# Kernel tuning notes

Measured on AMD Instinct MI355X. Metric: run time of the kernel, lower is better.

The kernel has to match this reference:

```python
import jax, jax.numpy as jnp
import numpy as np
import math

# B graphs of exactly NMAX nodes each
N, B, NMAX, E = 131072, 256, 512, 1048576
F_IN, C, H, HEADS, NUM_CLASSES = 128, 32, 64, 4, 2
K1 = 128  # ceil(avg_num_nodes * pooling_ratio) = ceil(512 * 0.25)
SCALE = math.sqrt(H)  # GMT MAB scales by sqrt(dim_V), not sqrt(head_dim)


def gcn_conv(x, W, b, src, dst, n):
    h = x @ W
    deg = jax.ops.segment_sum(jnp.ones(dst.shape[0], x.dtype), dst, num_segments=n) + 1.0
    dinv = jax.lax.rsqrt(deg)
    msg = h[src] * (dinv[src] * dinv[dst])[:, None]
    out = jax.ops.segment_sum(msg, dst, num_segments=n)
    out = out + h * (dinv * dinv)[:, None]  # self-loop term
    return out + b


def mab(Qin, K, V, addmask, Wq, bq, Wo, bo):
    # GMT multihead attention block (layer_norm=False)
    Q = Qin @ Wq + bq
    b_, nq, _ = Q.shape
    dh = H // HEADS
    q = Q.reshape(b_, nq, HEADS, dh)
    k = K.reshape(b_, K.shape[1], HEADS, dh)
    v = V.reshape(b_, K.shape[1], HEADS, dh)
    s = jnp.einsum('bqhd,bkhd->bhqk', q, k) / SCALE
    if addmask is not None:
        s = s + addmask[:, None, None, :]  # mask invalid keys
    A = jax.nn.softmax(s, axis=-1)
    o = jnp.einsum('bhqk,bkhd->bqhd', A, v).reshape(b_, nq, H)
    o = Q + o
    return o + jax.nn.relu(o @ Wo + bo)


def _forward(x0, conv1_W, conv1_b, conv2_W, conv2_b, conv3_W, conv3_b,
             pool_lin1_W, pool_lin1_b,
             pma1_S, pma1_Wq, pma1_bq, pma1_Wk, pma1_bk, pma1_Wv, pma1_bv, pma1_Wo, pma1_bo,
             sab_Wq, sab_bq, sab_Wk, sab_bk, sab_Wv, sab_bv, sab_Wo, sab_bo,
             pma2_S, pma2_Wq, pma2_bq, pma2_Wk, pma2_bk, pma2_Wv, pma2_bv, pma2_Wo, pma2_bo,
             pool_lin2_W, pool_lin2_b, lin1_W, lin1_b, lin2_W, lin2_b,
             edge_index, batch):
    src, dst = edge_index[0], edge_index[1]
    x1 = jax.nn.relu(gcn_conv(x0, conv1_W, conv1_b, src, dst, N))
    x2 = jax.nn.relu(gcn_conv(x1, conv2_W, conv2_b, src, dst, N))
    x3 = jax.nn.relu(gcn_conv(x2, conv3_W, conv3_b, src, dst, N))
    xc = jnp.concatenate([x1, x2, x3], axis=-1)         # [N, 96]
    xl = xc @ pool_lin1_W + pool_lin1_b                 # [N, H] (GMT lin1)

    # to_dense_batch bookkeeping (batch is sorted per graph)
    counts = jax.ops.segment_sum(jnp.ones(N, jnp.int32), batch, num_segments=B)
    starts = jnp.cumsum(counts) - counts
    pos = jnp.arange(N, dtype=jnp.int32) - starts[batch]
    valid = jnp.zeros((B, NMAX), bool).at[batch, pos].set(True)
    addmask = jnp.where(valid, 0.0, -1e9).astype(xl.dtype)

    def dense(h):
        return jnp.zeros((B, NMAX, h.shape[-1]), h.dtype).at[batch, pos].set(h)

    # GMPool_G: seed queries attend over GCNConv-transformed node features
    Kd = dense(gcn_conv(xl, pma1_Wk, pma1_bk, src, dst, N))
    Vd = dense(gcn_conv(xl, pma1_Wv, pma1_bv, src, dst, N))
    Q = jnp.broadcast_to(pma1_S[None], (B, K1, H))
    bx = mab(Q, Kd, Vd, addmask, pma1_Wq, pma1_bq, pma1_Wo, pma1_bo)

    # SelfAtt (mask=None after first pool)
    bx = mab(bx, bx @ sab_Wk + sab_bk, bx @ sab_Wv + sab_bv, None,
             sab_Wq, sab_bq, sab_Wo, sab_bo)

    # GMPool_I with single seed (last pool -> 1 output node per graph)
    Q2 = jnp.broadcast_to(pma2_S[None], (B, 1, H))
    bx = mab(Q2, bx @ pma2_Wk + pma2_bk, bx @ pma2_Wv + pma2_bv, None,
             pma2_Wq, pma2_bq, pma2_Wo, pma2_bo)

    g = bx[:, 0] @ pool_lin2_W + pool_lin2_b            # [B, 32] (GMT lin2)
    h1 = jax.nn.relu(g @ lin1_W + lin1_b)               # dropout identity in eval
    logits = h1 @ lin2_W + lin2_b
    return jax.nn.log_softmax(logits, axis=-1)


def setup_inputs() -> dict:
    key = jax.random.key(0)
    ks = iter(jax.random.split(key, 80))
    def Wm(fi, fo):
        return jax.random.normal(next(ks), (fi, fo), jnp.float32) / np.sqrt(fi)
    def bv(fo):
        return jax.random.normal(next(ks), (fo,), jnp.float32) * 0.01
    inp = {}
    inp['x0'] = jax.random.normal(next(ks), (N, F_IN), jnp.float32)
    g = jax.random.randint(next(ks), (E,), 0, B)
    so = jax.random.randint(next(ks), (E,), 0, NMAX)
    do = jax.random.randint(next(ks), (E,), 0, NMAX)
    inp['edge_index'] = jnp.stack([g * NMAX + so, g * NMAX + do]).astype(jnp.int32)
    inp['batch'] = jnp.arange(N, dtype=jnp.int32) // NMAX
    inp['conv1_W'], inp['conv1_b'] = Wm(F_IN, C), bv(C)
    inp['conv2_W'], inp['conv2_b'] = Wm(C, C), bv(C)
    inp['conv3_W'], inp['conv3_b'] = Wm(C, C), bv(C)
    inp['pool_lin1_W'], inp['pool_lin1_b'] = Wm(3 * C, H), bv(H)
    inp['pma1_S'] = jax.random.normal(next(ks), (K1, H), jnp.float32)
    for p in ['pma1', 'sab', 'pma2']:
        for nm in ['q', 'k', 'v', 'o']:
            inp[p + '_W' + nm], inp[p + '_b' + nm] = Wm(H, H), bv(H)
    inp['pma2_S'] = jax.random.normal(next(ks), (1, H), jnp.float32)
    inp['pool_lin2_W'], inp['pool_lin2_b'] = Wm(H, C), bv(C)
    inp['lin1_W'], inp['lin1_b'] = Wm(C, 16), bv(16)
    inp['lin2_W'], inp['lin2_b'] = Wm(16, NUM_CLASSES), bv(NUM_CLASSES)
    return inp


def reference(x0, edge_index, batch, conv1_W, conv1_b, conv2_W, conv2_b, conv3_W, conv3_b,
              pool_lin1_W, pool_lin1_b,
              pma1_S, pma1_Wq, pma1_bq, pma1_Wk, pma1_bk, pma1_Wv, pma1_bv, pma1_Wo, pma1_bo,
              sab_Wq, sab_bq, sab_Wk, sab_bk, sab_Wv, sab_bv, sab_Wo, sab_bo,
              pma2_S, pma2_Wq, pma2_bq, pma2_Wk, pma2_bk, pma2_Wv, pma2_bv, pma2_Wo, pma2_bo,
              pool_lin2_W, pool_lin2_b, lin1_W, lin1_b, lin2_W, lin2_b):
    return _forward(x0, conv1_W, conv1_b, conv2_W, conv2_b, conv3_W, conv3_b,
                    pool_lin1_W, pool_lin1_b,
                    pma1_S, pma1_Wq, pma1_bq, pma1_Wk, pma1_bk, pma1_Wv, pma1_bv, pma1_Wo, pma1_bo,
                    sab_Wq, sab_bq, sab_Wk, sab_bk, sab_Wv, sab_bv, sab_Wo, sab_bo,
                    pma2_S, pma2_Wq, pma2_bq, pma2_Wk, pma2_bk, pma2_Wv, pma2_bv, pma2_Wo, pma2_bo,
                    pool_lin2_W, pool_lin2_b, lin1_W, lin1_b, lin2_W, lin2_b,
                    edge_index, batch)
```

## Files before the change

### kernel.cpp

```cpp
#include <hip/hip_runtime.h>
#include <hip/hip_bf16.h>

#define N_NODES 131072
#define NGRAPH  256
#define NMAXN   512
#define NEDGE   1048576
#define FIN     128
#define HDIM    64
#define K1Q     128
#define EPB     1024
#define NBLK    (NEDGE / EPB)

__global__ __launch_bounds__(256) void k_hist2(const int* __restrict__ dst,
                                               int* __restrict__ h) {
    __shared__ int lh[NGRAPH];
    const int tid = threadIdx.x;
    lh[tid] = 0;
    __syncthreads();
    const int base = blockIdx.x * EPB;
#pragma unroll
    for (int j = 0; j < 4; ++j)
        atomicAdd(&lh[dst[base + j * 256 + tid] >> 9], 1);
    __syncthreads();
    h[blockIdx.x * 256 + tid] = lh[tid];
}

__global__ __launch_bounds__(256) void k_scan_bins(int* __restrict__ h,
                                                   int* __restrict__ binTot) {
    const int b = blockIdx.x;
    const int tid = threadIdx.x;
    int v[4], s = 0;
#pragma unroll
    for (int j = 0; j < 4; ++j) { v[j] = h[(tid * 4 + j) * 256 + b]; s += v[j]; }
    __shared__ int sc[256];
    sc[tid] = s;
    __syncthreads();
    for (int o = 1; o < 256; o <<= 1) {
        int t = (tid >= o) ? sc[tid - o] : 0;
        __syncthreads();
        sc[tid] += t;
        __syncthreads();
    }
    int run = sc[tid] - s;
#pragma unroll
    for (int j = 0; j < 4; ++j) { int t = v[j]; h[(tid * 4 + j) * 256 + b] = run; run += t; }
    if (tid == 255) binTot[b] = sc[255];
}

__global__ __launch_bounds__(256) void k_binstart(const int* __restrict__ binTot,
                                                  int* __restrict__ starts) {
    const int tid = threadIdx.x;
    int v = binTot[tid];
    __shared__ int sc[256];
    sc[tid] = v;
    __syncthreads();
    for (int o = 1; o < 256; o <<= 1) {
        int t = (tid >= o) ? sc[tid - o] : 0;
        __syncthreads();
        sc[tid] += t;
        __syncthreads();
    }
    starts[tid] = sc[tid] - v;
    if (tid == 255) starts[256] = sc[255];
}

__global__ __launch_bounds__(256) void k_scatter2(const int* __restrict__ src,
                                                  const int* __restrict__ dst,
                                                  const int* __restrict__ h,
                                                  const int* __restrict__ starts,
                                                  int* __restrict__ epack) {
    __shared__ int base[NGRAPH];
    const int tid = threadIdx.x;
    base[tid] = h[blockIdx.x * 256 + tid] + starts[tid];
    __syncthreads();
    const int b0 = blockIdx.x * EPB;
#pragma unroll
    for (int j = 0; j < 4; ++j) {
        int e = b0 + j * 256 + tid;
        int d = dst[e];
        int pos = atomicAdd(&base[d >> 9], 1);
        epack[pos] = ((src[e] & (NMAXN - 1)) << 9) | (d & (NMAXN - 1));
    }
}

__global__ __launch_bounds__(256) void k_sort_dst(
    const int* __restrict__ epack, const int* __restrict__ starts,
    int* __restrict__ esrc, int* __restrict__ rowptr)
{
    __shared__ int hist[NMAXN];
    __shared__ int excl[NMAXN];
    __shared__ int psc[256];
    const int g = blockIdx.x, tid = threadIdx.x;
    const int e0 = starts[g], e1 = starts[g + 1];
    hist[tid] = 0; hist[tid + 256] = 0;
    __syncthreads();
    for (int e = e0 + tid; e < e1; e += 256)
        atomicAdd(&hist[epack[e] & (NMAXN - 1)], 1);
    __syncthreads();
    int a = hist[2 * tid], b = hist[2 * tid + 1];
    psc[tid] = a + b;
    __syncthreads();
    for (int o = 1; o < 256; o <<= 1) {
        int t = (tid >= o) ? psc[tid - o] : 0;
        __syncthreads();
        psc[tid] += t;
        __syncthreads();
    }
    int ep = psc[tid] - a - b;
    excl[2 * tid] = ep;
    excl[2 * tid + 1] = ep + a;
    __syncthreads();
    rowptr[g * NMAXN + 2 * tid]     = e0 + excl[2 * tid];
    rowptr[g * NMAXN + 2 * tid + 1] = e0 + excl[2 * tid + 1];
    if (g == NGRAPH - 1 && tid == 0) rowptr[N_NODES] = NEDGE;
    __syncthreads();
    for (int e = e0 + tid; e < e1; e += 256) {
        int p = epack[e];
        int d = p & (NMAXN - 1);
        int pos = e0 + atomicAdd(&excl[d], 1);
        esrc[pos] = p >> 9;
    }
}

__global__ void k_dinv2(const int* __restrict__ rowptr, float* __restrict__ d) {
    int i = blockIdx.x * blockDim.x + threadIdx.x;
    if (i < N_NODES) d[i] = rsqrtf((float)(rowptr[i + 1] - rowptr[i]) + 1.0f);
}

template<int TM, int K, int CO, int MODE>
__global__ __launch_bounds__(256) void k_gemm(
    const float* __restrict__ A, int lda,
    const float* __restrict__ W, const float* __restrict__ bias,
    float* __restrict__ out, int ldo, int M)
{
    constexpr int WTS = K + 4;
    __shared__ float As[TM * K];
    __shared__ float Wt[CO * WTS];
    const int tid = threadIdx.x;
    const int row0 = blockIdx.x * TM;

    for (int i = tid; i < K * CO; i += 256) {
        int k = i / CO, c = i - k * CO;
        Wt[c * WTS + k] = W[i];
    }
    constexpr int VR = K / 4;
    for (int i = tid; i < TM * VR; i += 256) {
        int r = i / VR, v = i - r * VR;
        int gr = row0 + r;
        float4 val = make_float4(0.f, 0.f, 0.f, 0.f);
        if (gr < M) val = *(const float4*)(A + (size_t)gr * lda + v * 4);
        *(float4*)(As + r * K + v * 4) = val;
    }
    __syncthreads();

    constexpr int G = 256 / CO;
    constexpr int RPT = TM / G;
    const int co = tid % CO;
    const int g = tid / CO;

    float acc[RPT];
#pragma unroll
    for (int r = 0; r < RPT; ++r) acc[r] = 0.f;

    const float* wrow = Wt + co * WTS;
    for (int kk = 0; kk < K / 4; ++kk) {
        float4 w = *(const float4*)(wrow + kk * 4);
#pragma unroll
        for (int r = 0; r < RPT; ++r) {
            float4 a = *(const float4*)(As + (g * RPT + r) * K + kk * 4);
            acc[r] += a.x * w.x + a.y * w.y + a.z * w.z + a.w * w.w;
        }
    }
    float b = 0.f;
    if (MODE >= 1) b = bias[co];
#pragma unroll
    for (int r = 0; r < RPT; ++r) {
        int gr = row0 + g * RPT + r;
        if (gr < M) {
            float v = acc[r] + b;
            if (MODE == 2) v = fmaxf(v, 0.f);
            out[(size_t)gr * ldo + co] = v;
        }
    }
}

template<int RELU>
__global__ __launch_bounds__(256) void k_gcn_agg2(
    const float* __restrict__ T, int ldt,
    const float* __restrict__ dinv, const float* __restrict__ bias,
    const int* __restrict__ esrc, const int* __restrict__ rowptr,
    float* __restrict__ out, int ldo)
{
    constexpr int LS = 36;
    __shared__ float Tl[NMAXN * LS];
    __shared__ float dl[NMAXN];
    const int g = blockIdx.x;
    const int tid = threadIdx.x;
    const int node0 = g * NMAXN;

    for (int i = tid; i < NMAXN; i += 256) dl[i] = dinv[node0 + i];
    __syncthreads();
    for (int i = tid; i < NMAXN * 8; i += 256) {
        int r = i >> 3, c4 = (i & 7) << 2;
        float4 v = *(const float4*)(T + (size_t)(node0 + r) * ldt + c4);
        float w = dl[r];
        v.x *= w; v.y *= w; v.z *= w; v.w *= w;
        *(float4*)(Tl + r * LS + c4) = v;
    }
    __syncthreads();
    for (int i = tid; i < NMAXN * 8; i += 256) {
        int n = i >> 3, c4 = (i & 7) << 2;
        float4 acc = *(const float4*)(Tl + n * LS + c4);
        const int eb = rowptr[node0 + n], ee = rowptr[node0 + n + 1];
        for (int e = eb; e < ee; ++e) {
            int ls = esrc[e];
            const float4 v = *(const float4*)(Tl + ls * LS + c4);
            acc.x += v.x; acc.y += v.y; acc.z += v.z; acc.w += v.w;
        }
        float w = dl[n];
        float4 b4 = *(const float4*)(bias + c4);
        float4 o;
        o.x = b4.x + w * acc.x; o.y = b4.y + w * acc.y;
        o.z = b4.z + w * acc.z; o.w = b4.w + w * acc.w;
        if (RELU) {
            o.x = fmaxf(o.x, 0.f); o.y = fmaxf(o.y, 0.f);
            o.z = fmaxf(o.z, 0.f); o.w = fmaxf(o.w, 0.f);
        }
        *(float4*)(out + (size_t)(node0 + n) * ldo + c4) = o;
    }
}

template<int NK, bool QSH>
__global__ __launch_bounds__(256) void k_attn(
    const float* __restrict__ Q, const float* __restrict__ K,
    const float* __restrict__ V, float* __restrict__ O)
{
    constexpr int KH = NK / 2;
    __shared__ float Ks[NK * 16];
    __shared__ float Vs[NK * 16];
    __shared__ float Ml[128 * 18];
    const int g = blockIdx.x >> 2;
    const int h = blockIdx.x & 3;
    const int tid = threadIdx.x;
    for (int i = tid; i < NK * 4; i += 256) {
        int k = i >> 2, dc = (i & 3) << 2;
        const size_t off = ((size_t)g * NK + k) * HDIM + h * 16 + dc;
        *(float4*)(Ks + k * 16 + dc) = *(const float4*)(K + off);
        *(float4*)(Vs + k * 16 + dc) = *(const float4*)(V + off);
    }
    __syncthreads();
    const int q = tid & 127;
    const int half = tid >> 7;
    const int k0 = half * KH;
    const float* qp = QSH ? (Q + (size_t)q * HDIM + h * 16)
                          : (Q + ((size_t)g * K1Q + q) * HDIM + h * 16);
    float qv[16];
#pragma unroll
    for (int d = 0; d < 16; ++d) qv[d] = qp[d];

    float m = -1e30f, l = 0.f;
    float acc[16];
#pragma unroll
    for (int d = 0; d < 16; ++d) acc[d] = 0.f;

    for (int kt = 0; kt < KH; kt += 8) {
        const int kb = k0 + kt;
        float s[8];
#pragma unroll
        for (int j = 0; j < 8; ++j) {
            float t = 0.f;
#pragma unroll
            for (int d4 = 0; d4 < 4; ++d4) {
                float4 kv = *(const float4*)(Ks + (kb + j) * 16 + d4 * 4);
                t += qv[d4*4] * kv.x + qv[d4*4+1] * kv.y
                   + qv[d4*4+2] * kv.z + qv[d4*4+3] * kv.w;
            }
            s[j] = t * 0.125f;
        }
        float tmax = fmaxf(fmaxf(fmaxf(s[0], s[1]), fmaxf(s[2], s[3])),
                           fmaxf(fmaxf(s[4], s[5]), fmaxf(s[6], s[7])));
        if (tmax > m + 8.f) {
            float cr = __expf(m - tmax);
            l *= cr;
#pragma unroll
            for (int d = 0; d < 16; ++d) acc[d] *= cr;
            m = tmax;
        }
        float p[8];
#pragma unroll
        for (int j = 0; j < 8; ++j) { p[j] = __expf(s[j] - m); l += p[j]; }
#pragma unroll
        for (int d4 = 0; d4 < 4; ++d4) {
#pragma unroll
            for (int j = 0; j < 8; ++j) {
                float4 v = *(const float4*)(Vs + (kb + j) * 16 + d4 * 4);
                acc[d4*4]   += p[j] * v.x;
                acc[d4*4+1] += p[j] * v.y;
                acc[d4*4+2] += p[j] * v.z;
                acc[d4*4+3] += p[j] * v.w;
            }
        }
    }
    if (half) {
        float* w = Ml + q * 18;
        w[0] = m; w[1] = l;
#pragma unroll
        for (int d = 0; d < 16; ++d) w[2 + d] = acc[d];
    }
    __syncthreads();
    if (!half) {
        const float* r = Ml + q * 18;
        float m1 = r[0], l1 = r[1];
        float M = fmaxf(m, m1);
        float c0 = __expf(m - M), c1 = __expf(m1 - M);
        float inv = 1.f / (l * c0 + l1 * c1);
        float* op = O + ((size_t)g * K1Q + q) * HDIM + h * 16;
#pragma unroll
        for (int d = 0; d < 16; ++d) op[d] = (acc[d] * c0 + r[2 + d] * c1) * inv;
    }
}

__global__ __launch_bounds__(256) void k_attn_pma2(
    const float* __restrict__ Q2p, const float* __restrict__ K3,
    const float* __restrict__ V3, float* __restrict__ O3)
{
    const int t = threadIdx.x;
    const int lane = t & 63;
    const int g = blockIdx.x * 4 + (t >> 6);
    const float q = Q2p[lane];
    const float* Kg = K3 + (size_t)g * 128 * HDIM + lane;
    const float* Vg = V3 + (size_t)g * 128 * HDIM + lane;
    float m = -1e30f, l = 0.f, acc = 0.f;
    for (int k = 0; k < 128; ++k) {
        float s = q * Kg[(size_t)k * HDIM];
        s += __shfl_xor(s, 1); s += __shfl_xor(s, 2);
        s += __shfl_xor(s, 4); s += __shfl_xor(s, 8);
        s *= 0.125f;
        float mn = fmaxf(m, s);
        float cr = __expf(m - mn), p = __expf(s - mn);
        l = l * cr + p;
        acc = acc * cr + p * Vg[(size_t)k * HDIM];
        m = mn;
    }
    O3[(size_t)g * HDIM + lane] = acc / l;
}

template<int NQ>
__global__ __launch_bounds__(256) void k_mab_epi(
    const float* __restrict__ AO, const float* __restrict__ Qsrc,
    const float* __restrict__ W, const float* __restrict__ bias,
    float* __restrict__ out, int M)
{
    constexpr int TM = 128, KK = 64, CO = 64, WTS = KK + 4;
    __shared__ float Os[TM * KK];
    __shared__ float Wt[CO * WTS];
    const int tid = threadIdx.x;
    const int row0 = blockIdx.x * TM;
    for (int i = tid; i < KK * CO; i += 256) {
        int k = i >> 6, c = i & 63;
        Wt[c * WTS + k] = W[i];
    }
    for (int i = tid; i < TM * 16; i += 256) {
        int r = i >> 4, v = (i & 15) << 2;
        int gr = row0 + r;
        float4 a = make_float4(0.f, 0.f, 0.f, 0.f);
        if (gr < M) {
            float4 x = *(const float4*)(AO + (size_t)gr * KK + v);
            int qr = (NQ == 0) ? gr : (NQ == 1 ? 0 : (gr & (NQ - 1)));
            float4 qv = *(const float4*)(Qsrc + (size_t)qr * KK + v);
            a.x = x.x + qv.x; a.y = x.y + qv.y; a.z = x.z + qv.z; a.w = x.w + qv.w;
        }
        *(float4*)(Os + r * KK + v) = a;
    }
    __syncthreads();
    const int co = tid & 63, g = tid >> 6;
    float acc[32];
#pragma unroll
    for (int r = 0; r < 32; ++r) acc[r] = 0.f;
    const float* wrow = Wt + co * WTS;
    for (int kk = 0; kk < KK / 4; ++kk) {
        float4 w = *(const float4*)(wrow + kk * 4);
#pragma unroll
        for (int r = 0; r < 32; ++r) {
            float4 a = *(const float4*)(Os + (g * 32 + r) * KK + kk * 4);
            acc[r] += a.x * w.x + a.y * w.y + a.z * w.z + a.w * w.w;
        }
    }
    float b = bias[co];
#pragma unroll
    for (int r = 0; r < 32; ++r) {
        int gr = row0 + g * 32 + r;
        if (gr < M) {
            float o = Os[(g * 32 + r) * KK + co];
            out[(size_t)gr * CO + co] = o + fmaxf(acc[r] + b, 0.f);
        }
    }
}

__global__ __launch_bounds__(64) void k_head(
    const float* __restrict__ BX3,
    const float* __restrict__ W1, const float* __restrict__ b1,
    const float* __restrict__ W2, const float* __restrict__ b2,
    const float* __restrict__ W3, const float* __restrict__ b3,
    float* __restrict__ outp)
{
    __shared__ float w1[64 * 32], w2[32 * 16], w3[32], bb1[32], bb2[16], bb3[2];
    const int tid = threadIdx.x;
    for (int i = tid; i < 64 * 32; i += 64) w1[i] = W1[i];
    for (int i = tid; i < 32 * 16; i += 64) w2[i] = W2[i];
    if (tid < 32) { w3[tid] = W3[tid]; bb1[tid] = b1[tid]; }
    if (tid < 16) bb2[tid] = b2[tid];
    if (tid < 2)  bb3[tid] = b3[tid];
    __syncthreads();
    const int g = blockIdx.x * 64 + tid;
    float x[64];
#pragma unroll
    for (int v = 0; v < 16; ++v) {
        float4 t = *(const float4*)(BX3 + (size_t)g * 64 + v * 4);
        x[v*4] = t.x; x[v*4+1] = t.y; x[v*4+2] = t.z; x[v*4+3] = t.w;
    }
    float gv[32];
    for (int c = 0; c < 32; ++c) {
        float a = bb1[c];
        for (int k = 0; k < 64; ++k) a += x[k] * w1[k * 32 + c];
        gv[c] = a;
    }
    float h1[16];
    for (int c = 0; c < 16; ++c) {
        float a = bb2[c];
        for (int k = 0; k < 32; ++k) a += gv[k] * w2[k * 16 + c];
        h1[c] = fmaxf(a, 0.f);
    }
    float z0 = bb3[0], z1 = bb3[1];
    for (int k = 0; k < 16; ++k) { z0 += h1[k] * w3[k * 2]; z1 += h1[k] * w3[k * 2 + 1]; }
    float mm = fmaxf(z0, z1);
    float ls = mm + logf(__expf(z0 - mm) + __expf(z1 - mm));
    outp[g * 2]     = z0 - ls;
    outp[g * 2 + 1] = z1 - ls;
}

extern "C" void kernel_launch(void* const* d_in, const int* in_sizes, int n_in,
                              void* d_out, int out_size, void* d_ws, size_t ws_size,
                              hipStream_t stream) {
    const float* x0  = (const float*)d_in[0];
    const int*   ei  = (const int*)d_in[1];
    const float* c1W = (const float*)d_in[3];  const float* c1b = (const float*)d_in[4];
    const float* c2W = (const float*)d_in[5];  const float* c2b = (const float*)d_in[6];
    const float* c3W = (const float*)d_in[7];  const float* c3b = (const float*)d_in[8];
    const float* plW = (const float*)d_in[9];  const float* plb = (const float*)d_in[10];
    const float* S1  = (const float*)d_in[11];
    const float* p1Wq = (const float*)d_in[12]; const float* p1bq = (const float*)d_in[13];
    const float* p1Wk = (const float*)d_in[14]; const float* p1bk = (const float*)d_in[15];
    const float* p1Wv = (const float*)d_in[16]; const float* p1bv = (const float*)d_in[17];
    const float* p1Wo = (const float*)d_in[18]; const float* p1bo = (const float*)d_in[19];
    const float* sWq  = (const float*)d_in[20]; const float* sbq  = (const float*)d_in[21];
    const float* sWk  = (const float*)d_in[22]; const float* sbk  = (const float*)d_in[23];
    const float* sWv  = (const float*)d_in[24]; const float* sbv  = (const float*)d_in[25];
    const float* sWo  = (const float*)d_in[26]; const float* sbo  = (const float*)d_in[27];
    const float* p2Wq = (const float*)d_in[28]; const float* p2bq = (const float*)d_in[29];
    const float* p2Wk = (const float*)d_in[30]; const float* p2bk = (const float*)d_in[31];
    const float* p2Wv = (const float*)d_in[32]; const float* p2bv = (const float*)d_in[33];
    const float* p2Wo = (const float*)d_in[34]; const float* p2bo = (const float*)d_in[35];
    const float* S2   = (const float*)d_in[36];
    const float* pl2W = (const float*)d_in[37]; const float* pl2b = (const float*)d_in[38];
    const float* l1W  = (const float*)d_in[39]; const float* l1b  = (const float*)d_in[40];
    const float* l2W  = (const float*)d_in[41]; const float* l2b  = (const float*)d_in[42];

    const int* src = ei;
    const int* dst = ei + NEDGE;

    float* ws = (float*)d_ws;
    float* dinv = ws;
    size_t off = N_NODES;
    int* epack  = (int*)(ws + off); off += NEDGE;
    int* h      = (int*)(ws + off); off += NBLK * 256;
    int* binTot = (int*)(ws + off); off += 256;
    int* starts = (int*)(ws + off); off += 257;
    int* esrc   = (int*)(ws + off); off += NEDGE;
    int* rowptr = (int*)(ws + off); off += N_NODES + 1;
    off = (off + 255) & ~(size_t)255;
    float* Qp  = ws + off; off += K1Q * HDIM;
    float* Q2p = ws + off; off += HDIM;
    float* O3  = ws + off; off += NGRAPH * HDIM;
    float* BX3 = ws + off; off += NGRAPH * HDIM;
    off = (off + 1023) & ~(size_t)1023;
    float* P0 = ws + off;
    const size_t SL = (size_t)N_NODES * 32;
    float* T32 = P0;
    float* T64 = P0;
    float* XC  = P0 + 2 * SL;
    float* XL  = P0 + 5 * SL;
    float* KD  = P0 + 2 * SL;
    float* VD  = P0 + 5 * SL;
    float* O1  = P0 + 4 * SL;
    float* BX1 = P0 + 4 * SL + SL / 2;
    float* Qs  = P0;
    float* Ks_ = P0 + SL / 2;
    float* Vs_ = P0 + SL;
    float* O2  = P0 + SL + SL / 2;
    float* BX2 = P0 + 2 * SL;
    float* K3  = P0 + 2 * SL + SL / 2;
    float* V3  = P0 + 3 * SL;

    k_hist2<<<NBLK, 256, 0, stream>>>(dst, h);
    k_scan_bins<<<256, 256, 0, stream>>>(h, binTot);
    k_binstart<<<1, 256, 0, stream>>>(binTot, starts);
    k_scatter2<<<NBLK, 256, 0, stream>>>(src, dst, h, starts, epack);
    k_sort_dst<<<NGRAPH, 256, 0, stream>>>(epack, starts, esrc, rowptr);
    k_dinv2<<<512, 256, 0, stream>>>(rowptr, dinv);

    k_gemm<64, 128, 32, 0><<<2048, 256, 0, stream>>>(x0, FIN, c1W, nullptr, T32, 32, N_NODES);
    k_gcn_agg2<1><<<256, 256, 0, stream>>>(T32, 32, dinv, c1b, esrc, rowptr, XC, 96);
    k_gemm<128, 32, 32, 0><<<1024, 256, 0, stream>>>(XC, 96, c2W, nullptr, T32, 32, N_NODES);
    k_gcn_agg2<1><<<256, 256, 0, stream>>>(T32, 32, dinv, c2b, esrc, rowptr, XC + 32, 96);
    k_gemm<128, 32, 32, 0><<<1024, 256, 0, stream>>>(XC + 32, 96, c3W, nullptr, T32, 32, N_NODES);
    k_gcn_agg2<1><<<256, 256, 0, stream>>>(T32, 32, dinv, c3b, esrc, rowptr, XC + 64, 96);

    k_gemm<64, 96, 64, 1><<<2048, 256, 0, stream>>>(XC, 96, plW, plb, XL, 64, N_NODES);

    k_gemm<128, 64, 64, 0><<<1024, 256, 0, stream>>>(XL, 64, p1Wk, nullptr, T64, 64, N_NODES);
    k_gcn_agg2<0><<<256, 256, 0, stream>>>(T64, 64, dinv, p1bk, esrc, rowptr, KD, 64);
    k_gcn_agg2<0><<<256, 256, 0, stream>>>(T64 + 32, 64, dinv, p1bk + 32, esrc, rowptr, KD + 32, 64);
    k_gemm<128, 64, 64, 0><<<1024, 256, 0, stream>>>(XL, 64, p1Wv, nullptr, T64, 64, N_NODES);
    k_gcn_agg2<0><<<256, 256, 0, stream>>>(T64, 64, dinv, p1bv, esrc, rowptr, VD, 64);
    k_gcn_agg2<0><<<256, 256, 0, stream>>>(T64 + 32, 64, dinv, p1bv + 32, esrc, rowptr, VD + 32, 64);

    k_gemm<128, 64, 64, 1><<<1, 256, 0, stream>>>(S1, 64, p1Wq, p1bq, Qp, 64, K1Q);
    k_attn<512, true><<<NGRAPH * 4, 256, 0, stream>>>(Qp, KD, VD, O1);
    k_mab_epi<128><<<256, 256, 0, stream>>>(O1, Qp, p1Wo, p1bo, BX1, NGRAPH * K1Q);

    k_gemm<128, 64, 64, 1><<<256, 256, 0, stream>>>(BX1, 64, sWq, sbq, Qs, 64, NGRAPH * K1Q);
    k_gemm<128, 64, 64, 1><<<256, 256, 0, stream>>>(BX1, 64, sWk, sbk, Ks_, 64, NGRAPH * K1Q);
    k_gemm<128, 64, 64, 1><<<256, 256, 0, stream>>>(BX1, 64, sWv, sbv, Vs_, 64, NGRAPH * K1Q);
    k_attn<128, false><<<NGRAPH * 4, 256, 0, stream>>>(Qs, Ks_, Vs_, O2);
    k_mab_epi<0><<<256, 256, 0, stream>>>(O2, Qs, sWo, sbo, BX2, NGRAPH * K1Q);

    k_gemm<128, 64, 64, 1><<<256, 256, 0, stream>>>(BX2, 64, p2Wk, p2bk, K3, 64, NGRAPH * K1Q);
    k_gemm<128, 64, 64, 1><<<256, 256, 0, stream>>>(BX2, 64, p2Wv, p2bv, V3, 64, NGRAPH * K1Q);
    k_gemm<128, 64, 64, 1><<<1, 256, 0, stream>>>(S2, 64, p2Wq, p2bq, Q2p, 64, 1);
    k_attn_pma2<<<64, 256, 0, stream>>>(Q2p, K3, V3, O3);
    k_mab_epi<1><<<2, 256, 0, stream>>>(O3, Q2p, p2Wo, p2bo, BX3, NGRAPH);

    k_head<<<4, 64, 0, stream>>>(BX3, pl2W, pl2b, l1W, l1b, l2W, l2b,
                                 (float*)d_out);
}
```

Before: 1.182 ms.

## Fuse GCN feature GEMM into per-graph aggregation and split attention keys four ways

Replaces the separate node-feature GEMM plus aggregation kernels with one per-graph kernel. It stages the input rows and transposed weights in shared memory, computes the 32-column projection in registers, then aggregates over neighbours from shared memory. This removes the round trip of the intermediate T tensor through global memory and several launches. The attention kernel now splits keys into four quarters, with each thread handling two queries and a four-way merge that reuses the K buffer when it is large enough. The costs are a 64-entry register accumulator that may hurt occupancy, and only 256 blocks for the fused GEMM work.

```diff
diff --git a/kernel.cpp b/kernel.cpp
--- a/kernel.cpp
+++ b/kernel.cpp
@@ -184,44 +184,79 @@
     }
 }
 
-template<int RELU>
-__global__ __launch_bounds__(256) void k_gcn_agg2(
-    const float* __restrict__ T, int ldt,
-    const float* __restrict__ dinv, const float* __restrict__ bias,
+template<int K, int RELU>
+__global__ __launch_bounds__(256) void k_gcn_fused(
+    const float* __restrict__ A, int lda,
+    const float* __restrict__ W, int ldw,
+    const float* __restrict__ bias,
+    const float* __restrict__ dinv,
     const int* __restrict__ esrc, const int* __restrict__ rowptr,
     float* __restrict__ out, int ldo)
 {
-    constexpr int LS = 36;
-    __shared__ float Tl[NMAXN * LS];
+    constexpr int C   = 8192 / K;
+    constexpr int NCH = NMAXN / C;
+    constexpr int RPT = C / 8;
+    constexpr int LS  = 36;
+    constexpr int WTS = K + 4;
+    __shared__ float U[NMAXN * LS];
     __shared__ float dl[NMAXN];
-    const int g = blockIdx.x;
-    const int tid = threadIdx.x;
+    float* As = U;
+    float* Wt = U + 8192;
+    const int g = blockIdx.x, tid = threadIdx.x;
     const int node0 = g * NMAXN;
 
+    for (int i = tid; i < 32 * K; i += 256) {
+        int k = i >> 5, co = i & 31;
+        Wt[co * WTS + k] = W[k * ldw + co];
+    }
     for (int i = tid; i < NMAXN; i += 256) dl[i] = dinv[node0 + i];
-    __syncthreads();
-    for (int i = tid; i < NMAXN * 8; i += 256) {
-        int r = i >> 3, c4 = (i & 7) << 2;
-        float4 v = *(const float4*)(T + (size_t)(node0 + r) * ldt + c4);
-        float w = dl[r];
-        v.x *= w; v.y *= w; v.z *= w; v.w *= w;
-        *(float4*)(Tl + r * LS + c4) = v;
-    }
+
+    const int co = tid & 31, grp = tid >> 5;
+    float acc[64];
+#pragma unroll
+    for (int r = 0; r < 64; ++r) acc[r] = 0.f;
+
+#pragma unroll
+    for (int ch = 0; ch < NCH; ++ch) {
+        __syncthreads();
+        for (int i = tid; i < C * (K / 4); i += 256) {
+            int r = i / (K / 4), v = i % (K / 4);
+            *(float4*)(As + r * K + v * 4) =
+                *(const float4*)(A + (size_t)(node0 + ch * C + r) * lda + v * 4);
+        }
+        __syncthreads();
+        for (int kk = 0; kk < K / 4; ++kk) {
+            float4 w = *(const float4*)(Wt + co * WTS + kk * 4);
+#pragma unroll
+            for (int r = 0; r < RPT; ++r) {
+                float4 a = *(const float4*)(As + (grp * RPT + r) * K + kk * 4);
+                acc[ch * RPT + r] += a.x * w.x + a.y * w.y + a.z * w.z + a.w * w.w;
+            }
+        }
+    }
+    __syncthreads();
+    float* Tl = U;
+#pragma unroll
+    for (int ch = 0; ch < NCH; ++ch)
+#pragma unroll
+        for (int r = 0; r < RPT; ++r) {
+            int row = ch * C + grp * RPT + r;
+            Tl[row * LS + co] = acc[ch * RPT + r] * dl[row];
+        }
     __syncthreads();
     for (int i = tid; i < NMAXN * 8; i += 256) {
         int n = i >> 3, c4 = (i & 7) << 2;
-        float4 acc = *(const float4*)(Tl + n * LS + c4);
+        float4 s = *(const float4*)(Tl + n * LS + c4);
         const int eb = rowptr[node0 + n], ee = rowptr[node0 + n + 1];
         for (int e = eb; e < ee; ++e) {
-            int ls = esrc[e];
-            const float4 v = *(const float4*)(Tl + ls * LS + c4);
-            acc.x += v.x; acc.y += v.y; acc.z += v.z; acc.w += v.w;
-        }
-        float w = dl[n];
+            const float4 v = *(const float4*)(Tl + esrc[e] * LS + c4);
+            s.x += v.x; s.y += v.y; s.z += v.z; s.w += v.w;
+        }
+        float wv = dl[n];
         float4 b4 = *(const float4*)(bias + c4);
         float4 o;
-        o.x = b4.x + w * acc.x; o.y = b4.y + w * acc.y;
-        o.z = b4.z + w * acc.z; o.w = b4.w + w * acc.w;
+        o.x = b4.x + wv * s.x; o.y = b4.y + wv * s.y;
+        o.z = b4.z + wv * s.z; o.w = b4.w + wv * s.w;
         if (RELU) {
             o.x = fmaxf(o.x, 0.f); o.y = fmaxf(o.y, 0.f);
             o.z = fmaxf(o.z, 0.f); o.w = fmaxf(o.w, 0.f);
@@ -235,10 +270,12 @@
     const float* __restrict__ Q, const float* __restrict__ K,
     const float* __restrict__ V, float* __restrict__ O)
 {
-    constexpr int KH = NK / 2;
+    constexpr int KQ  = NK / 4;
+    constexpr int MLF = 3 * 128 * 18;
     __shared__ float Ks[NK * 16];
     __shared__ float Vs[NK * 16];
-    __shared__ float Ml[128 * 18];
+    __shared__ float Mlsep[(NK * 16 >= MLF) ? 4 : MLF];
+    float* Ml = (NK * 16 >= MLF) ? Ks : Mlsep;
     const int g = blockIdx.x >> 2;
     const int h = blockIdx.x & 3;
     const int tid = threadIdx.x;
@@ -249,74 +286,111 @@
         *(float4*)(Vs + k * 16 + dc) = *(const float4*)(V + off);
     }
     __syncthreads();
-    const int q = tid & 127;
-    const int half = tid >> 7;
-    const int k0 = half * KH;
-    const float* qp = QSH ? (Q + (size_t)q * HDIM + h * 16)
-                          : (Q + ((size_t)g * K1Q + q) * HDIM + h * 16);
-    float qv[16];
-#pragma unroll
-    for (int d = 0; d < 16; ++d) qv[d] = qp[d];
-
-    float m = -1e30f, l = 0.f;
-    float acc[16];
-#pragma unroll
-    for (int d = 0; d < 16; ++d) acc[d] = 0.f;
-
-    for (int kt = 0; kt < KH; kt += 8) {
+    const int qs = tid & 63;
+    const int quarter = tid >> 6;
+    const int k0 = quarter * KQ;
+    const float* qp0 = QSH ? (Q + (size_t)qs * HDIM + h * 16)
+                           : (Q + ((size_t)g * K1Q + qs) * HDIM + h * 16);
+    const float* qp1 = qp0 + 64 * HDIM;
+    float qv0[16], qv1[16];
+#pragma unroll
+    for (int d = 0; d < 16; ++d) { qv0[d] = qp0[d]; qv1[d] = qp1[d]; }
+
+    float m0 = -1e30f, l0 = 0.f, m1 = -1e30f, l1 = 0.f;
+    float acc0[16], acc1[16];
+#pragma unroll
+    for (int d = 0; d < 16; ++d) { acc0[d] = 0.f; acc1[d] = 0.f; }
+
+    for (int kt = 0; kt < KQ; kt += 8) {
         const int kb = k0 + kt;
-        float s[8];
+        float s0[8], s1[8];
 #pragma unroll
         for (int j = 0; j < 8; ++j) {
-            float t = 0.f;
+            float t0 = 0.f, t1 = 0.f;
 #pragma unroll
             for (int d4 = 0; d4 < 4; ++d4) {
                 float4 kv = *(const float4*)(Ks + (kb + j) * 16 + d4 * 4);
-                t += qv[d4*4] * kv.x + qv[d4*4+1] * kv.y
-                   + qv[d4*4+2] * kv.z + qv[d4*4+3] * kv.w;
+                t0 += qv0[d4*4] * kv.x + qv0[d4*4+1] * kv.y
+                    + qv0[d4*4+2] * kv.z + qv0[d4*4+3] * kv.w;
+                t1 += qv1[d4*4] * kv.x + qv1[d4*4+1] * kv.y
+                    + qv1[d4*4+2] * kv.z + qv1[d4*4+3] * kv.w;
             }
-            s[j] = t * 0.125f;
-        }
-        float tmax = fmaxf(fmaxf(fmaxf(s[0], s[1]), fmaxf(s[2], s[3])),
-                           fmaxf(fmaxf(s[4], s[5]), fmaxf(s[6], s[7])));
-        if (tmax > m + 8.f) {
-            float cr = __expf(m - tmax);
-            l *= cr;
-#pragma unroll
-            for (int d = 0; d < 16; ++d) acc[d] *= cr;
-            m = tmax;
-        }
-        float p[8];
-#pragma unroll
-        for (int j = 0; j < 8; ++j) { p[j] = __expf(s[j] - m); l += p[j]; }
+            s0[j] = t0 * 0.125f; s1[j] = t1 * 0.125f;
+        }
+        float tm0 = fmaxf(fmaxf(fmaxf(s0[0], s0[1]), fmaxf(s0[2], s0[3])),
+                          fmaxf(fmaxf(s0[4], s0[5]), fmaxf(s0[6], s0[7])));
+        float tm1 = fmaxf(fmaxf(fmaxf(s1[0], s1[1]), fmaxf(s1[2], s1[3])),
+                          fmaxf(fmaxf(s1[4], s1[5]), fmaxf(s1[6], s1[7])));
+        if (tm0 > m0 + 8.f) {
+            float cr = __expf(m0 - tm0);
+            l0 *= cr;
+#pragma unroll
+            for (int d = 0; d < 16; ++d) acc0[d] *= cr;
+            m0 = tm0;
+        }
+        if (tm1 > m1 + 8.f) {
+            float cr = __expf(m1 - tm1);
+            l1 *= cr;
+#pragma unroll
+            for (int d = 0; d < 16; ++d) acc1[d] *= cr;
+            m1 = tm1;
+        }
+        float p0[8], p1[8];
+#pragma unroll
+        for (int j = 0; j < 8; ++j) {
+            p0[j] = __expf(s0[j] - m0); l0 += p0[j];
+            p1[j] = __expf(s1[j] - m1); l1 += p1[j];
+        }
 #pragma unroll
         for (int d4 = 0; d4 < 4; ++d4) {
 #pragma unroll
             for (int j = 0; j < 8; ++j) {
                 float4 v = *(const float4*)(Vs + (kb + j) * 16 + d4 * 4);
-                acc[d4*4]   += p[j] * v.x;
-                acc[d4*4+1] += p[j] * v.y;
-                acc[d4*4+2] += p[j] * v.z;
-                acc[d4*4+3] += p[j] * v.w;
+                acc0[d4*4]   += p0[j] * v.x;  acc1[d4*4]   += p1[j] * v.x;
+                acc0[d4*4+1] += p0[j] * v.y;  acc1[d4*4+1] += p1[j] * v.y;
+                acc0[d4*4+2] += p0[j] * v.z;  acc1[d4*4+2] += p1[j] * v.z;
+                acc0[d4*4+3] += p0[j] * v.w;  acc1[d4*4+3] += p1[j] * v.w;
             }
         }
     }
-    if (half) {
-        float* w = Ml + q * 18;
-        w[0] = m; w[1] = l;
-#pragma unroll
-        for (int d = 0; d < 16; ++d) w[2 + d] = acc[d];
-    }
-    __syncthreads();
-    if (!half) {
-        const float* r = Ml + q * 18;
-        float m1 = r[0], l1 = r[1];
-        float M = fmaxf(m, m1);
-        float c0 = __expf(m - M), c1 = __expf(m1 - M);
-        float inv = 1.f / (l * c0 + l1 * c1);
-        float* op = O + ((size_t)g * K1Q + q) * HDIM + h * 16;
-#pragma unroll
-        for (int d = 0; d < 16; ++d) op[d] = (acc[d] * c0 + r[2 + d] * c1) * inv;
+    __syncthreads();
+    if (quarter) {
+        float* w0 = Ml + ((quarter - 1) * 128 + qs) * 18;
+        float* w1 = Ml + ((quarter - 1) * 128 + qs + 64) * 18;
+        w0[0] = m0; w0[1] = l0;
+        w1[0] = m1; w1[1] = l1;
+#pragma unroll
+        for (int d = 0; d < 16; ++d) { w0[2 + d] = acc0[d]; w1[2 + d] = acc1[d]; }
+    }
+    __syncthreads();
+    if (quarter == 0) {
+#pragma unroll
+        for (int qq = 0; qq < 2; ++qq) {
+            const int q = qs + qq * 64;
+            float m = qq ? m1 : m0, l = qq ? l1 : l0;
+            float ac[16];
+#pragma unroll
+            for (int d = 0; d < 16; ++d) ac[d] = qq ? acc1[d] : acc0[d];
+            float M = m;
+#pragma unroll
+            for (int p = 0; p < 3; ++p) M = fmaxf(M, Ml[(p * 128 + q) * 18]);
+            float c = __expf(m - M);
+            float L = l * c;
+#pragma unroll
+            for (int d = 0; d < 16; ++d) ac[d] *= c;
+#pragma unroll
+            for (int p = 0; p < 3; ++p) {
+                const float* r = Ml + (p * 128 + q) * 18;
+                float cp = __expf(r[0] - M);
+                L += r[1] * cp;
+#pragma unroll
+                for (int d = 0; d < 16; ++d) ac[d] += r[2 + d] * cp;
+            }
+            float inv = 1.f / L;
+            float* op = O + ((size_t)g * K1Q + q) * HDIM + h * 16;
+#pragma unroll
+            for (int d = 0; d < 16; ++d) op[d] = ac[d] * inv;
+        }
     }
 }
 
@@ -486,12 +560,10 @@
     off = (off + 1023) & ~(size_t)1023;
     float* P0 = ws + off;
     const size_t SL = (size_t)N_NODES * 32;
-    float* T32 = P0;
-    float* T64 = P0;
     float* XC  = P0 + 2 * SL;
     float* XL  = P0 + 5 * SL;
-    float* KD  = P0 + 2 * SL;
-    float* VD  = P0 + 5 * SL;
+    float* KD  = P0;
+    float* VD  = P0 + 2 * SL;
     float* O1  = P0 + 4 * SL;
     float* BX1 = P0 + 4 * SL + SL / 2;
     float* Qs  = P0;
@@ -509,21 +581,16 @@
     k_sort_dst<<<NGRAPH, 256, 0, stream>>>(epack, starts, esrc, rowptr);
     k_dinv2<<<512, 256, 0, stream>>>(rowptr, dinv);
 
-    k_gemm<64, 128, 32, 0><<<2048, 256, 0, stream>>>(x0, FIN, c1W, nullptr, T32, 32, N_NODES);
-    k_gcn_agg2<1><<<256, 256, 0, stream>>>(T32, 32, dinv, c1b, esrc, rowptr, XC, 96);
-    k_gemm<128, 32, 32, 0><<<1024, 256, 0, stream>>>(XC, 96, c2W, nullptr, T32, 32, N_NODES);
-    k_gcn_agg2<1><<<256, 256, 0, stream>>>(T32, 32, dinv, c2b, esrc, rowptr, XC + 32, 96);
-    k_gemm<128, 32, 32, 0><<<1024, 256, 0, stream>>>(XC + 32, 96, c3W, nullptr, T32, 32, N_NODES);
-    k_gcn_agg2<1><<<256, 256, 0, stream>>>(T32, 32, dinv, c3b, esrc, rowptr, XC + 64, 96);
+    k_gcn_fused<128, 1><<<NGRAPH, 256, 0, stream>>>(x0, FIN, c1W, 32, c1b, dinv, esrc, rowptr, XC, 96);
+    k_gcn_fused<32, 1><<<NGRAPH, 256, 0, stream>>>(XC, 96, c2W, 32, c2b, dinv, esrc, rowptr, XC + 32, 96);
+    k_gcn_fused<32, 1><<<NGRAPH, 256, 0, stream>>>(XC + 32, 96, c3W, 32, c3b, dinv, esrc, rowptr, XC + 64, 96);
 
     k_gemm<64, 96, 64, 1><<<2048, 256, 0, stream>>>(XC, 96, plW, plb, XL, 64, N_NODES);
 
-    k_gemm<128, 64, 64, 0><<<1024, 256, 0, stream>>>(XL, 64, p1Wk, nullptr, T64, 64, N_NODES);
-    k_gcn_agg2<0><<<256, 256, 0, stream>>>(T64, 64, dinv, p1bk, esrc, rowptr, KD, 64);
-    k_gcn_agg2<0><<<256, 256, 0, stream>>>(T64 + 32, 64, dinv, p1bk + 32, esrc, rowptr, KD + 32, 64);
-    k_gemm<128, 64, 64, 0><<<1024, 256, 0, stream>>>(XL, 64, p1Wv, nullptr, T64, 64, N_NODES);
-    k_gcn_agg2<0><<<256, 256, 0, stream>>>(T64, 64, dinv, p1bv, esrc, rowptr, VD, 64);
-    k_gcn_agg2<0><<<256, 256, 0, stream>>>(T64 + 32, 64, dinv, p1bv + 32, esrc, rowptr, VD + 32, 64);
+    k_gcn_fused<64, 0><<<NGRAPH, 256, 0, stream>>>(XL, 64, p1Wk, 64, p1bk, dinv, esrc, rowptr, KD, 64);
+    k_gcn_fused<64, 0><<<NGRAPH, 256, 0, stream>>>(XL, 64, p1Wk + 32, 64, p1bk + 32, dinv, esrc, rowptr, KD + 32, 64);
+    k_gcn_fused<64, 0><<<NGRAPH, 256, 0, stream>>>(XL, 64, p1Wv, 64, p1bv, dinv, esrc, rowptr, VD, 64);
+    k_gcn_fused<64, 0><<<NGRAPH, 256, 0, stream>>>(XL, 64, p1Wv + 32, 64, p1bv + 32, dinv, esrc, rowptr, VD + 32, 64);
 
     k_gemm<128, 64, 64, 1><<<1, 256, 0, stream>>>(S1, 64, p1Wq, p1bq, Qp, 64, K1Q);
     k_attn<512, true><<<NGRAPH * 4, 256, 0, stream>>>(Qp, KD, VD, O1);
```

Result: slower. 1.339 ms (+13.3%).
